# Kernel tuning notes

Measured on AMD Instinct MI355X. Metric: run time of the kernel, lower is better.

Reference implementation:

```python
import jax, jax.numpy as jnp
import numpy as np

DIM = 192          # out_dim
HEADS = 8          # num_heads (split into 2 branches of 4)
SS = (4, 8)        # split_size
B, HH, WW, CIN = 8, 128, 128, 192


def calc_mask(H, W, wh, ww):
    # Swin-style shift mask for windows of (wh, ww), shift (wh//2, ww//2).
    sh, sw = wh // 2, ww // 2
    h = jnp.arange(H)
    w = jnp.arange(W)
    hreg = (h >= H - wh).astype(jnp.int32) + (h >= H - sh).astype(jnp.int32)
    wreg = (w >= W - ww).astype(jnp.int32) + (w >= W - sw).astype(jnp.int32)
    img = hreg[:, None] * 3 + wreg[None, :]                      # (H, W) region ids
    win = img.reshape(H // wh, wh, W // ww, ww).transpose(0, 2, 1, 3).reshape(-1, wh * ww)
    return jnp.where(win[:, :, None] != win[:, None, :], -100.0, 0.0)  # (nW, N, N)


def window_attention(q, k, v, mask, d, Hsp, Wsp):
    # q,k,v: (B, C, H, W); mask: (u*v, N, N); d heads, window Hsp x Wsp
    Bc, C, H, W = k.shape
    u, vv = H // Hsp, W // Wsp
    c = C // d
    N = Hsp * Wsp
    scale = c ** -0.5

    def v2w(t):  # 'b (d c) (u h) (v w) -> (b u v) d (h w) c'
        return t.reshape(Bc, d, c, u, Hsp, vv, Wsp).transpose(0, 3, 5, 1, 4, 6, 2).reshape(Bc * u * vv, d, N, c)

    qw, kw, vw = v2w(q), v2w(k), v2w(v)
    attn = jnp.einsum('ndic,ndjc->ndij', qw, kw) * scale          # (B*u*v, d, N, N)
    attn = attn.reshape(Bc, u * vv, d, N, N) + mask[None, :, None, :, :]
    a = jax.nn.softmax(attn, axis=-1).reshape(Bc * u * vv, d, N, N)
    o = jnp.einsum('ndij,ndjc->ndic', a, vw)
    # '(b u v) d (h w) c -> b (d c) (u h) (v w)'
    return o.reshape(Bc, u, vv, d, Hsp, Wsp, c).transpose(0, 3, 6, 1, 4, 2, 5).reshape(Bc, C, H, W)


def setup_inputs() -> dict:
    key = jax.random.key(0)
    k0, k1, k2, k3 = jax.random.split(key, 4)
    x = jax.random.normal(k0, (B, HH * WW, CIN), dtype=jnp.float32)
    Wq = jax.random.normal(k1, (CIN, DIM), dtype=jnp.float32) * 0.02
    Wkv = jax.random.normal(k2, (CIN, 2 * DIM), dtype=jnp.float32) * 0.02
    Wproj = jax.random.normal(k3, (DIM, DIM), dtype=jnp.float32) * 0.02
    bproj = jnp.zeros((DIM,), dtype=jnp.float32)
    return {"x": x, "Wq": Wq, "Wkv": Wkv, "Wproj": Wproj, "bproj": bproj, "H": HH, "W": WW}


def reference(x, Wq, Wkv, Wproj, bproj, H, W):
    Bc, L, _ = x.shape
    C = Wq.shape[1]
    q = (x @ Wq).reshape(Bc, H, W, C).transpose(0, 3, 1, 2)       # (B, C, H, W)
    kv = (x @ Wkv).reshape(Bc, H, W, 2, C)
    k = kv[..., 0, :].transpose(0, 3, 1, 2)
    v = kv[..., 1, :].transpose(0, 3, 1, 2)

    Ch = C // 2
    s0, s1 = SS[0] // 2, SS[1] // 2
    roll0 = lambda t: jnp.roll(t, (-s0, -s1), axis=(-2, -1))
    roll1 = lambda t: jnp.roll(t, (-s1, -s0), axis=(-2, -1))
    mask0 = calc_mask(H, W, SS[0], SS[1])   # branch 0: 4x8 windows
    mask1 = calc_mask(H, W, SS[1], SS[0])   # branch 1: 8x4 windows
    d = HEADS // 2

    x0 = window_attention(roll0(q[:, :Ch]), roll0(k[:, :Ch]), roll0(v[:, :Ch]), mask0, d, SS[0], SS[1])
    x1 = window_attention(roll1(q[:, Ch:]), roll1(k[:, Ch:]), roll1(v[:, Ch:]), mask1, d, SS[1], SS[0])
    x0 = jnp.roll(x0, (s0, s1), axis=(-2, -1))
    x1 = jnp.roll(x1, (s1, s0), axis=(-2, -1))

    out = jnp.concatenate([x0, x1], axis=1)                        # (B, C, H, W)
    out = out.transpose(0, 2, 3, 1).reshape(Bc, L, C)
    return out @ Wproj + bproj
```

## Files before the change

### kernel.cpp

```cpp
#include <hip/hip_runtime.h>
#include <hip/hip_bf16.h>
#include <stdint.h>

typedef __bf16 bf16;
typedef __bf16 bf16x8 __attribute__((ext_vector_type(8)));
typedef __bf16 bf16x4 __attribute__((ext_vector_type(4)));
typedef float  f32x4  __attribute__((ext_vector_type(4)));

#define MROWS 131072

__device__ __forceinline__ f32x4 mfma16(bf16x8 a, bf16x8 b, f32x4 c) {
    return __builtin_amdgcn_mfma_f32_16x16x32_bf16(a, b, c, 0, 0, 0);
}
__device__ __forceinline__ f32x4 zero4() {
    f32x4 z; z[0]=0.f; z[1]=0.f; z[2]=0.f; z[3]=0.f; return z;
}
__device__ __forceinline__ bf16x8 zero8() {
    bf16x8 z;
#pragma unroll
    for (int i = 0; i < 8; ++i) z[i] = (bf16)0.f;
    return z;
}

__global__ void kw_transpose(const float* __restrict__ Wq, const float* __restrict__ Wkv,
                             const float* __restrict__ Wp, bf16* __restrict__ Wt,
                             bf16* __restrict__ Wpt) {
    int col = blockIdx.x;
    int k = threadIdx.x;
    if (col < 192)      Wt[col * 192 + k] = (bf16)Wq[k * 192 + col];
    else if (col < 576) Wt[col * 192 + k] = (bf16)Wkv[k * 384 + (col - 192)];
    else                Wpt[(col - 576) * 192 + k] = (bf16)Wp[k * 192 + (col - 576)];
}

__global__ __launch_bounds__(256, 3) void kfused(const float* __restrict__ X,
                                                 const bf16* __restrict__ Wt,
                                                 bf16* __restrict__ Out) {
    const int branch = blockIdx.y;
    const int bw = blockIdx.x;
    const int img = bw >> 9;
    const int widx = bw & 511;
    const int wh = branch ? 8 : 4, ww = branch ? 4 : 8;
    const int lww = branch ? 2 : 3;
    const int lnv = branch ? 5 : 4;
    const int sh = wh >> 1, sw = ww >> 1;
    const int wa = widx >> lnv;
    const int wb = widx & ((128 >> lww) - 1);

    __shared__ int pix[32];
    __shared__ int rid[32];
    __shared__ __align__(16) bf16 xs[32][200];
    __shared__ __align__(16) bf16 qs[32][104];
    __shared__ __align__(16) bf16 kss[32][104];
    __shared__ bf16 vt[4][24][40];
    __shared__ bf16 pl[4][32][40];
    __shared__ __align__(16) bf16 ob[32][104];

    const int tid = threadIdx.x;
    if (tid < 32) {
        int ih = tid >> lww, iw = tid & (ww - 1);
        int hh = wa * wh + ih, wp = wb * ww + iw;
        int hreg = (hh >= 128 - wh) + (hh >= 128 - sh);
        int wreg = (wp >= 128 - ww) + (wp >= 128 - sw);
        rid[tid] = hreg * 3 + wreg;
        int srh = (hh + sh) & 127, srw = (wp + sw) & 127;
        pix[tid] = img * 16384 + srh * 128 + srw;
    }
    __syncthreads();

#pragma unroll
    for (int i = 0; i < 6; ++i) {
        int c = tid + i * 256;
        int row = c / 48, c4 = (c % 48) * 4;
        f32x4 f = *(const f32x4*)(X + (size_t)pix[row] * 192 + c4);
        bf16x4 h;
#pragma unroll
        for (int e = 0; e < 4; ++e) h[e] = (bf16)f[e];
        *(bf16x4*)&xs[row][c4] = h;
    }
    __syncthreads();

    const int hd = tid >> 6;
    const int l = tid & 63, li = l & 15, lk = l >> 4;

    bf16x8 xf[2][6];
#pragma unroll
    for (int mt = 0; mt < 2; ++mt)
#pragma unroll
        for (int ks = 0; ks < 6; ++ks)
            xf[mt][ks] = *(const bf16x8*)&xs[mt * 16 + li][ks * 32 + lk * 8];

#pragma unroll
    for (int j = 0; j < 5; ++j) {
        int nt = hd + 4 * j;
        if (nt < 18) {
            int seg = nt / 6;
            int cwi = (nt % 6) * 16;
            const bf16* wrow = Wt + (size_t)(seg * 192 + branch * 96 + cwi + li) * 192 + lk * 8;
            bf16x8 bfr[6];
#pragma unroll
            for (int ks = 0; ks < 6; ++ks) bfr[ks] = *(const bf16x8*)(wrow + ks * 32);
            f32x4 a0 = zero4(), a1 = zero4();
#pragma unroll
            for (int ks = 0; ks < 6; ++ks) {
                a0 = mfma16(bfr[ks], xf[0][ks], a0);
                a1 = mfma16(bfr[ks], xf[1][ks], a1);
            }
            if (seg < 2) {
                bf16* dst = (seg == 0) ? &qs[0][0] : &kss[0][0];
                bf16x4 p0, p1;
#pragma unroll
                for (int r = 0; r < 4; ++r) { p0[r] = (bf16)a0[r]; p1[r] = (bf16)a1[r]; }
                *(bf16x4*)(dst + li * 104 + cwi + lk * 4) = p0;
                *(bf16x4*)(dst + (16 + li) * 104 + cwi + lk * 4) = p1;
            } else {
#pragma unroll
                for (int r = 0; r < 4; ++r) {
                    int vc = cwi + lk * 4 + r;
                    vt[vc / 24][vc % 24][li] = (bf16)a0[r];
                    vt[vc / 24][vc % 24][16 + li] = (bf16)a1[r];
                }
            }
        }
    }
    __syncthreads();

    bf16x8 aq[2], bk[2];
#pragma unroll
    for (int t = 0; t < 2; ++t) {
        if (lk < 3) {
            aq[t] = *(const bf16x8*)&qs[t * 16 + li][hd * 24 + lk * 8];
            bk[t] = *(const bf16x8*)&kss[t * 16 + li][hd * 24 + lk * 8];
        } else {
            aq[t] = zero8();
            bk[t] = zero8();
        }
    }
    f32x4 s[2][2];
#pragma unroll
    for (int it = 0; it < 2; ++it)
#pragma unroll
        for (int jt = 0; jt < 2; ++jt) s[it][jt] = mfma16(aq[it], bk[jt], zero4());

    const float scale = 0.2041241452319315f;
    const int r0 = lk * 4;
    const int rj0 = rid[li], rj1 = rid[16 + li];
#pragma unroll
    for (int it = 0; it < 2; ++it) {
#pragma unroll
        for (int r = 0; r < 4; ++r) {
            int i = it * 16 + r0 + r;
            int ri = rid[i];
            float v0 = s[it][0][r] * scale + ((ri != rj0) ? -100.f : 0.f);
            float v1 = s[it][1][r] * scale + ((ri != rj1) ? -100.f : 0.f);
            float m = fmaxf(v0, v1);
#pragma unroll
            for (int d = 1; d < 16; d <<= 1) m = fmaxf(m, __shfl_xor(m, d));
            float e0 = __expf(v0 - m), e1 = __expf(v1 - m);
            float sm = e0 + e1;
#pragma unroll
            for (int d = 1; d < 16; d <<= 1) sm += __shfl_xor(sm, d);
            float inv = 1.f / sm;
            pl[hd][i][li] = (bf16)(e0 * inv);
            pl[hd][i][16 + li] = (bf16)(e1 * inv);
        }
    }
    __syncthreads();

    bf16x8 ap[2], bv[2];
#pragma unroll
    for (int it = 0; it < 2; ++it)
        ap[it] = *(const bf16x8*)(&pl[hd][it * 16 + li][lk * 8]);
#pragma unroll
    for (int ct = 0; ct < 2; ++ct) {
        int col = ct * 16 + li;
        if (col > 23) col = 23;
        bv[ct] = *(const bf16x8*)(&vt[hd][col][lk * 8]);
    }
    f32x4 o[2][2];
#pragma unroll
    for (int it = 0; it < 2; ++it)
#pragma unroll
        for (int ct = 0; ct < 2; ++ct) o[it][ct] = mfma16(ap[it], bv[ct], zero4());

#pragma unroll
    for (int it = 0; it < 2; ++it)
#pragma unroll
        for (int ct = 0; ct < 2; ++ct) {
            int col = ct * 16 + li;
            if (col < 24) {
#pragma unroll
                for (int r = 0; r < 4; ++r)
                    ob[it * 16 + r0 + r][hd * 24 + col] = (bf16)o[it][ct][r];
            }
        }
    __syncthreads();
    for (int c = tid; c < 384; c += 256) {
        int row = c / 12, ch = c % 12;
        *(bf16x8*)(Out + (size_t)pix[row] * 192 + branch * 96 + ch * 8) =
            *(const bf16x8*)&ob[row][ch * 8];
    }
}

#define BSTR 200
__global__ __launch_bounds__(256, 4) void kproj(const bf16* __restrict__ Ab,
                                                const bf16* __restrict__ Wpt,
                                                const float* __restrict__ bias,
                                                float* __restrict__ Out) {
    __shared__ __align__(16) bf16 Bs[96][BSTR];
    const int lid = blockIdx.x;
    const int xcd = lid & 7, s = lid >> 3;
    const int mg = xcd * 128 + s / 2;
    const int nb = s & 1;
    const int tid = threadIdx.x;
    const int w = tid >> 6, l = tid & 63, li = l & 15, lk = l >> 4;
    const int rb = mg * 128 + w * 32;
    const int cb = nb * 96;

    bf16x8 a[2][6];
#pragma unroll
    for (int it = 0; it < 2; ++it)
#pragma unroll
        for (int ks = 0; ks < 6; ++ks)
            a[it][ks] = *(const bf16x8*)(Ab + (size_t)(rb + it * 16 + li) * 192 + ks * 32 + lk * 8);

#pragma unroll
    for (int i = 0; i < 9; ++i) {
        int c = i * 256 + tid;
        int r = c / 24, col = (c % 24) * 8;
        *(bf16x8*)&Bs[r][col] = *(const bf16x8*)(Wpt + (size_t)(cb + r) * 192 + col);
    }
    __syncthreads();

    f32x4 acc[2][6];
#pragma unroll
    for (int it = 0; it < 2; ++it)
#pragma unroll
        for (int nt = 0; nt < 6; ++nt) acc[it][nt] = zero4();

#pragma unroll
    for (int nt = 0; nt < 6; ++nt) {
#pragma unroll
        for (int ks = 0; ks < 6; ++ks) {
            bf16x8 b = *(const bf16x8*)&Bs[nt * 16 + li][ks * 32 + lk * 8];
            acc[0][nt] = mfma16(b, a[0][ks], acc[0][nt]);
            acc[1][nt] = mfma16(b, a[1][ks], acc[1][nt]);
        }
    }

#pragma unroll
    for (int nt = 0; nt < 6; ++nt) {
        f32x4 bv4 = *(const f32x4*)(bias + cb + nt * 16 + lk * 4);
#pragma unroll
        for (int it = 0; it < 2; ++it) {
            f32x4 ov = acc[it][nt];
#pragma unroll
            for (int r = 0; r < 4; ++r) ov[r] += bv4[r];
            *(f32x4*)(Out + (size_t)(rb + it * 16 + li) * 192 + cb + nt * 16 + lk * 4) = ov;
        }
    }
}

extern "C" void kernel_launch(void* const* d_in, const int* in_sizes, int n_in,
                              void* d_out, int out_size, void* d_ws, size_t ws_size,
                              hipStream_t stream) {
    const float* x    = (const float*)d_in[0];
    const float* Wq   = (const float*)d_in[1];
    const float* Wkv  = (const float*)d_in[2];
    const float* Wp   = (const float*)d_in[3];
    const float* bias = (const float*)d_in[4];
    float* out = (float*)d_out;

    bf16* Ab  = (bf16*)d_ws;
    bf16* Wt  = Ab + (size_t)MROWS * 192;
    bf16* Wpt = Wt + 576 * 192;

    hipLaunchKernelGGL(kw_transpose, dim3(768), dim3(192), 0, stream, Wq, Wkv, Wp, Wt, Wpt);
    hipLaunchKernelGGL(kfused, dim3(4096, 2), dim3(256), 0, stream, x, Wt, Ab);
    hipLaunchKernelGGL(kproj, dim3(2048), dim3(256), 0, stream, Ab, Wpt, bias, out);
}
```

Before: 156.7 us.

## Alias shared buffers, prefetch weight fragments, raise kfused occupancy to four blocks

Overlays the shared-memory buffers that are never live at the same time (xs with pl, qs with ob), which shrinks LDS per block, and raises the launch bound from 3 to 4 blocks per CU. Each thread now computes source pixel offsets inline instead of reading them from the shared pix array, so the first barrier can go. The QKV projection loop double-buffers the weight fragment loads, fetching the next tile before issuing MFMAs on the current one. The aim is more blocks in flight and hidden global weight-load latency, at the cost of extra registers that may spill under the tighter occupancy bound.

```diff
diff --git a/kernel.cpp b/kernel.cpp
--- a/kernel.cpp
+++ b/kernel.cpp
@@ -32,7 +32,7 @@
     else                Wpt[(col - 576) * 192 + k] = (bf16)Wp[k * 192 + (col - 576)];
 }
 
-__global__ __launch_bounds__(256, 3) void kfused(const float* __restrict__ X,
+__global__ __launch_bounds__(256, 4) void kfused(const float* __restrict__ X,
                                                  const bf16* __restrict__ Wt,
                                                  bf16* __restrict__ Out) {
     const int branch = blockIdx.y;
@@ -46,14 +46,15 @@
     const int wa = widx >> lnv;
     const int wb = widx & ((128 >> lww) - 1);
 
+    __shared__ __align__(16) char smem[33792];
+    bf16 (*xs)[200]    = (bf16(*)[200])smem;
+    bf16 (*pl)[32][40] = (bf16(*)[32][40])smem;
+    bf16 (*qs)[104]    = (bf16(*)[104])(smem + 12800);
+    bf16 (*ob)[104]    = (bf16(*)[104])(smem + 12800);
+    bf16 (*kss)[104]   = (bf16(*)[104])(smem + 19456);
+    bf16 (*vt)[24][40] = (bf16(*)[24][40])(smem + 26112);
     __shared__ int pix[32];
     __shared__ int rid[32];
-    __shared__ __align__(16) bf16 xs[32][200];
-    __shared__ __align__(16) bf16 qs[32][104];
-    __shared__ __align__(16) bf16 kss[32][104];
-    __shared__ bf16 vt[4][24][40];
-    __shared__ bf16 pl[4][32][40];
-    __shared__ __align__(16) bf16 ob[32][104];
 
     const int tid = threadIdx.x;
     if (tid < 32) {
@@ -65,13 +66,16 @@
         int srh = (hh + sh) & 127, srw = (wp + sw) & 127;
         pix[tid] = img * 16384 + srh * 128 + srw;
     }
-    __syncthreads();
 
 #pragma unroll
     for (int i = 0; i < 6; ++i) {
         int c = tid + i * 256;
         int row = c / 48, c4 = (c % 48) * 4;
-        f32x4 f = *(const f32x4*)(X + (size_t)pix[row] * 192 + c4);
+        int ih = row >> lww, iw = row & (ww - 1);
+        int hh = wa * wh + ih, wp = wb * ww + iw;
+        int srh = (hh + sh) & 127, srw = (wp + sw) & 127;
+        size_t px = (size_t)(img * 16384 + srh * 128 + srw);
+        f32x4 f = *(const f32x4*)(X + px * 192 + c4);
         bf16x4 h;
 #pragma unroll
         for (int e = 0; e < 4; ++e) h[e] = (bf16)f[e];
@@ -89,37 +93,55 @@
         for (int ks = 0; ks < 6; ++ks)
             xf[mt][ks] = *(const bf16x8*)&xs[mt * 16 + li][ks * 32 + lk * 8];
 
-#pragma unroll
-    for (int j = 0; j < 5; ++j) {
-        int nt = hd + 4 * j;
-        if (nt < 18) {
-            int seg = nt / 6;
-            int cwi = (nt % 6) * 16;
-            const bf16* wrow = Wt + (size_t)(seg * 192 + branch * 96 + cwi + li) * 192 + lk * 8;
-            bf16x8 bfr[6];
-#pragma unroll
-            for (int ks = 0; ks < 6; ++ks) bfr[ks] = *(const bf16x8*)(wrow + ks * 32);
-            f32x4 a0 = zero4(), a1 = zero4();
-#pragma unroll
-            for (int ks = 0; ks < 6; ++ks) {
-                a0 = mfma16(bfr[ks], xf[0][ks], a0);
-                a1 = mfma16(bfr[ks], xf[1][ks], a1);
+#define LOADW(dst, nt) {                                                            \
+        int seg_ = (nt) / 6, cwi_ = ((nt) % 6) * 16;                                \
+        const bf16* wr = Wt + (size_t)(seg_ * 192 + branch * 96 + cwi_ + li) * 192  \
+                            + lk * 8;                                               \
+        _Pragma("unroll")                                                           \
+        for (int ks = 0; ks < 6; ++ks) dst[ks] = *(const bf16x8*)(wr + ks * 32);    \
+    }
+#define MFMA_SCATTER(frag, nt) {                                                    \
+        f32x4 a0 = zero4(), a1 = zero4();                                           \
+        _Pragma("unroll")                                                           \
+        for (int ks = 0; ks < 6; ++ks) {                                            \
+            a0 = mfma16(frag[ks], xf[0][ks], a0);                                   \
+            a1 = mfma16(frag[ks], xf[1][ks], a1);                                   \
+        }                                                                           \
+        int seg_ = (nt) / 6, cwi_ = ((nt) % 6) * 16;                                \
+        if (seg_ < 2) {                                                             \
+            bf16 (*dst)[104] = (seg_ == 0) ? qs : kss;                              \
+            bf16x4 p0, p1;                                                          \
+            _Pragma("unroll")                                                       \
+            for (int r = 0; r < 4; ++r) { p0[r] = (bf16)a0[r]; p1[r] = (bf16)a1[r]; } \
+            *(bf16x4*)&dst[li][cwi_ + lk * 4] = p0;                                 \
+            *(bf16x4*)&dst[16 + li][cwi_ + lk * 4] = p1;                            \
+        } else {                                                                    \
+            _Pragma("unroll")                                                       \
+            for (int r = 0; r < 4; ++r) {                                           \
+                int vc = cwi_ + lk * 4 + r;                                         \
+                vt[vc / 24][vc % 24][li] = (bf16)a0[r];                             \
+                vt[vc / 24][vc % 24][16 + li] = (bf16)a1[r];                        \
+            }                                                                       \
+        }                                                                           \
+    }
+
+    {
+        bf16x8 cur[6], nxt[6];
+        LOADW(cur, hd);
+#pragma unroll
+        for (int j = 0; j < 4; ++j) {
+            int nt = hd + 4 * j;
+            if (j < 3) {
+                LOADW(nxt, nt + 4);
+            } else if (hd < 2) {
+                LOADW(nxt, nt + 4);
             }
-            if (seg < 2) {
-                bf16* dst = (seg == 0) ? &qs[0][0] : &kss[0][0];
-                bf16x4 p0, p1;
-#pragma unroll
-                for (int r = 0; r < 4; ++r) { p0[r] = (bf16)a0[r]; p1[r] = (bf16)a1[r]; }
-                *(bf16x4*)(dst + li * 104 + cwi + lk * 4) = p0;
-                *(bf16x4*)(dst + (16 + li) * 104 + cwi + lk * 4) = p1;
-            } else {
-#pragma unroll
-                for (int r = 0; r < 4; ++r) {
-                    int vc = cwi + lk * 4 + r;
-                    vt[vc / 24][vc % 24][li] = (bf16)a0[r];
-                    vt[vc / 24][vc % 24][16 + li] = (bf16)a1[r];
-                }
-            }
+            MFMA_SCATTER(cur, nt);
+#pragma unroll
+            for (int ks = 0; ks < 6; ++ks) cur[ks] = nxt[ks];
+        }
+        if (hd < 2) {
+            MFMA_SCATTER(cur, hd + 16);
         }
     }
     __syncthreads();
@@ -199,6 +221,8 @@
         *(bf16x8*)(Out + (size_t)pix[row] * 192 + branch * 96 + ch * 8) =
             *(const bf16x8*)&ob[row][ch * 8];
     }
+#undef LOADW
+#undef MFMA_SCATTER
 }
 
 #define BSTR 200
```

New measurement: 148.2 us. 5.5% less time.
